# Kernel tuning notes

Measured on AMD Instinct MI355X. Metric: run time of the kernel, lower is better.

Reference implementation:

```python
import jax, jax.numpy as jnp
import numpy as np

B, S, HID = 2, 2048, 1024
NH, HD = 16, 64  # num heads, head dim
NEG = 1e10

def setup_inputs() -> dict:
    key = jax.random.key(0)
    ks = jax.random.split(key, 4)
    scale = 1.0 / np.sqrt(HID)
    return {
        "hidden_states": jax.random.normal(ks[0], (B, S, HID), jnp.float32),
        "attention_mask": jnp.zeros((B, 1, 1, S), jnp.float32),
        "Wq": jax.random.normal(ks[1], (HID, HID), jnp.float32) * scale,
        "bq": jnp.zeros((HID,), jnp.float32),
        "Wk": jax.random.normal(ks[2], (HID, HID), jnp.float32) * scale,
        "bk": jnp.zeros((HID,), jnp.float32),
        "Wv": jax.random.normal(ks[3], (HID, HID), jnp.float32) * scale,
        "bv": jnp.zeros((HID,), jnp.float32),
    }

def _split_heads(x):
    # [B,S,HID] -> [B,NH,S,HD]
    return x.reshape(B, S, NH, HD).transpose(0, 2, 1, 3)

def reference(hidden_states, attention_mask, Wq, bq, Wk, bk, Wv, bv):
    q = _split_heads(hidden_states @ Wq.T + bq)
    k = _split_heads(hidden_states @ Wk.T + bk)
    v = _split_heads(hidden_states @ Wv.T + bv)
    scores = jnp.einsum("bhqd,bhkd->bhqk", q, k) / np.sqrt(HD)
    causal = jnp.tril(jnp.ones((S, S), jnp.float32))  # [S,S]
    scores = scores * causal - NEG * (1.0 - causal)
    scores = scores + attention_mask
    probs = jax.nn.softmax(scores, axis=-1)  # [B,NH,S,S]
    ctx = jnp.einsum("bhqk,bhkd->bhqd", probs, v)
    ctx = ctx.transpose(0, 2, 1, 3).reshape(B, S, HID)
    return (ctx, probs)
```

## Files before the change

kernel.cpp:

```cpp
#include <hip/hip_runtime.h>

#define S_LEN 2048
#define HIDN  1024
#define NHEAD 16
#define HDIM  64
#define NBATCH 2

typedef __bf16 bf16x8 __attribute__((ext_vector_type(8)));
typedef float  f32x4  __attribute__((ext_vector_type(4)));
typedef unsigned int  u32x4 __attribute__((ext_vector_type(4)));
typedef unsigned short u16;
typedef unsigned short u16x4 __attribute__((ext_vector_type(4)));

#define LOG2E      1.4426950408889634f
#define QS_L2E     0.18033688011112042f
#define NEG8_L2E  -11.541560327111707f

#define PSTR 68

__device__ __forceinline__ u16 f2bf(float f) {
    union { float f; unsigned int u; } v; v.f = f;
    unsigned int u = v.u;
    unsigned int r = ((u >> 16) & 1u) + 0x7FFFu;
    return (u16)((u + r) >> 16);
}

__device__ __forceinline__ f32x4 mfma16(bf16x8 a, bf16x8 b, f32x4 c) {
    return __builtin_amdgcn_mfma_f32_16x16x32_bf16(a, b, c, 0, 0, 0);
}

__device__ __forceinline__ f32x4 zf4() { f32x4 z = {0.f, 0.f, 0.f, 0.f}; return z; }

__device__ __forceinline__ bf16x8 pack8_trunc(f32x4 a, f32x4 b) {
    union { f32x4 f; u32x4 u; } ua, ub;
    ua.f = a; ub.f = b;
    union { unsigned int d[4]; bf16x8 v; } r;
    r.d[0] = __builtin_amdgcn_perm(ua.u.y, ua.u.x, 0x07060302u);
    r.d[1] = __builtin_amdgcn_perm(ua.u.w, ua.u.z, 0x07060302u);
    r.d[2] = __builtin_amdgcn_perm(ub.u.y, ub.u.x, 0x07060302u);
    r.d[3] = __builtin_amdgcn_perm(ub.u.w, ub.u.z, 0x07060302u);
    return r.v;
}

__device__ __forceinline__ void gld16(void* lds, const void* g) {
    __builtin_amdgcn_global_load_lds(
        (const __attribute__((address_space(1))) void*)g,
        (__attribute__((address_space(3))) void*)lds, 16, 0, 0);
}

__global__ __launch_bounds__(256) void cvt_bf16(
    const float* __restrict__ s, u16* __restrict__ d, int n)
{
    int i = (blockIdx.x * 256 + threadIdx.x) * 4;
    if (i >= n) return;
    float4 v = *(const float4*)&s[i];
    u16x4 o = { f2bf(v.x), f2bf(v.y), f2bf(v.z), f2bf(v.w) };
    *(u16x4*)&d[i] = o;
}

__global__ __launch_bounds__(256) void qkv_gemm(
    const u16* __restrict__ hsb,
    const u16* __restrict__ Wqb, const u16* __restrict__ Wkb, const u16* __restrict__ Wvb,
    const float* __restrict__ bq, const float* __restrict__ bk, const float* __restrict__ bv,
    u16* __restrict__ Qf, u16* __restrict__ Kf, u16* __restrict__ Vt)
{
    __shared__ u16 As[128 * 32];
    __shared__ u16 Bs[128 * 32];

    const int z = blockIdx.z;
    const u16*   __restrict__ W    = (z == 0) ? Wqb : (z == 1) ? Wkb : Wvb;
    const float* __restrict__ bias = (z == 0) ? bq  : (z == 1) ? bk  : bv;

    const int mbase = blockIdx.x * 128;
    const int nbase = blockIdx.y * 128;
    const int tid  = threadIdx.x;
    const int lane = tid & 63;
    const int wv   = tid >> 6;
    const int wrow = wv >> 1, wcol = wv & 1;
    const int lrow = lane & 15, quad = lane >> 4;

    const int c0 = tid, c1 = tid + 256;
    const int r0 = c0 >> 2, o0 = (c0 & 3) * 8;
    const int r1 = c1 >> 2, o1 = (c1 & 3) * 8;
    const u16* a0p = &hsb[(size_t)(mbase + r0) * HIDN + o0];
    const u16* a1p = &hsb[(size_t)(mbase + r1) * HIDN + o1];
    const u16* b0p = &W  [(size_t)(nbase + r0) * HIDN + o0];
    const u16* b1p = &W  [(size_t)(nbase + r1) * HIDN + o1];

    f32x4 acc[4][4];
#pragma unroll
    for (int i = 0; i < 4; ++i)
#pragma unroll
        for (int j = 0; j < 4; ++j) acc[i][j] = zf4();

    for (int k0 = 0; k0 < HIDN; k0 += 32) {
        gld16(&As[c0 * 8], a0p + k0);
        gld16(&As[c1 * 8], a1p + k0);
        gld16(&Bs[c0 * 8], b0p + k0);
        gld16(&Bs[c1 * 8], b1p + k0);
        __syncthreads();

        bf16x8 af[4], bfr[4];
#pragma unroll
        for (int i = 0; i < 4; ++i)
            af[i] = *(const bf16x8*)&As[(wrow * 64 + i * 16 + lrow) * 32 + quad * 8];
#pragma unroll
        for (int j = 0; j < 4; ++j)
            bfr[j] = *(const bf16x8*)&Bs[(wcol * 64 + j * 16 + lrow) * 32 + quad * 8];
#pragma unroll
        for (int i = 0; i < 4; ++i)
#pragma unroll
            for (int j = 0; j < 4; ++j)
                acc[i][j] = mfma16(af[i], bfr[j], acc[i][j]);
        __syncthreads();
    }

    if (z == 2) {
        const int bb = mbase >> 11;
        const int sb = mbase & 2047;
#pragma unroll
        for (int i = 0; i < 4; ++i) {
#pragma unroll
            for (int j = 0; j < 4; ++j) {
                const int n = nbase + wcol * 64 + j * 16 + lrow;
                const int hh = n >> 6, d = n & 63;
                const float bs = bias[n];
                const int sbase = sb + wrow * 64 + i * 16 + quad * 4;
                u16x4 pk = { f2bf(acc[i][j][0] + bs), f2bf(acc[i][j][1] + bs),
                             f2bf(acc[i][j][2] + bs), f2bf(acc[i][j][3] + bs) };
                *(u16x4*)&Vt[(((size_t)(bb * NHEAD + hh)) * HDIM + d) * S_LEN + sbase] = pk;
            }
        }
    } else {
        u16* __restrict__ O = (z == 0) ? Qf : Kf;
#pragma unroll
        for (int i = 0; i < 4; ++i) {
#pragma unroll
            for (int j = 0; j < 4; ++j) {
                const int n = nbase + wcol * 64 + j * 16 + lrow;
                const float bs = bias[n];
#pragma unroll
                for (int reg = 0; reg < 4; ++reg) {
                    const int m = mbase + wrow * 64 + i * 16 + quad * 4 + reg;
                    O[(size_t)m * HIDN + n] = f2bf(acc[i][j][reg] + bs);
                }
            }
        }
    }
}

__global__ __launch_bounds__(256) void attn_kernel(
    const u16* __restrict__ Qf,
    const u16* __restrict__ Kf,
    const u16* __restrict__ Vt,
    const float* __restrict__ amask,
    float* __restrict__ ctx,
    float* __restrict__ probs)
{
    const int qt = 127 - blockIdx.x;
    const int h  = blockIdx.y;
    const int b  = blockIdx.z;
    const int bh = b * NHEAD + h;
    const int tid  = threadIdx.x;
    const int lane = tid & 63;
    const int wv   = tid >> 6;
    const int lrow = lane & 15, quad = lane >> 4;
    const int row0 = qt * 16;
    const int dti  = qt >> 2;
    const int nkt  = dti + 1;

    __shared__ float pfl[4][16 * PSTR];
    __shared__ float l_sh[4][16];

    {
        const int tail  = nkt * 64;
        const int nt4   = (S_LEN - tail) >> 2;
        const int r  = tid >> 4;
        const int c0 = tid & 15;
        const f32x4 zf = {0.f, 0.f, 0.f, 0.f};
        float* pr = &probs[((size_t)bh * S_LEN + row0 + r) * S_LEN + tail];
        for (int c4 = c0; c4 < nt4; c4 += 16)
            __builtin_nontemporal_store(zf, (f32x4*)&pr[c4 * 4]);
    }

    const u16* qp = &Qf[((size_t)b * S_LEN + row0 + lrow) * HIDN + h * HDIM + quad * 8];
    const bf16x8 qa0 = *(const bf16x8*)qp;
    const bf16x8 qa1 = *(const bf16x8*)(qp + 32);

    const float* __restrict__ am = &amask[(size_t)b * S_LEN];
    const u16* __restrict__ kbase = &Kf[(size_t)b * S_LEN * HIDN + h * HDIM + quad * 8];

    float l_lane[4] = {0.f, 0.f, 0.f, 0.f};
    for (int kt = wv; kt < nkt; kt += 4) {
        f32x4 c[4];
#pragma unroll
        for (int cb = 0; cb < 4; ++cb) {
            const int col = kt * 64 + cb * 16 + lrow;
            const u16* kp = kbase + (size_t)col * HIDN;
            bf16x8 kb0 = *(const bf16x8*)kp;
            bf16x8 kb1 = *(const bf16x8*)(kp + 32);
            c[cb] = mfma16(qa0, kb0, zf4());
            c[cb] = mfma16(qa1, kb1, c[cb]);
        }
        if (kt == dti) {
#pragma unroll
            for (int cb = 0; cb < 4; ++cb) {
                const int col = kt * 64 + cb * 16 + lrow;
                const float m8 = fmaf(am[col], LOG2E, NEG8_L2E);
#pragma unroll
                for (int reg = 0; reg < 4; ++reg) {
                    const int row = row0 + quad * 4 + reg;
                    const float e = exp2f(fmaf(c[cb][reg], QS_L2E, m8));
                    l_lane[reg] += (col <= row) ? e : 0.f;
                }
            }
        } else {
#pragma unroll
            for (int cb = 0; cb < 4; ++cb) {
                const int col = kt * 64 + cb * 16 + lrow;
                const float m8 = fmaf(am[col], LOG2E, NEG8_L2E);
#pragma unroll
                for (int reg = 0; reg < 4; ++reg)
                    l_lane[reg] += exp2f(fmaf(c[cb][reg], QS_L2E, m8));
            }
        }
    }
#pragma unroll
    for (int reg = 0; reg < 4; ++reg) {
#pragma unroll
        for (int off = 1; off < 16; off <<= 1)
            l_lane[reg] += __shfl_xor(l_lane[reg], off, 16);
    }
    if (lrow == 0) {
#pragma unroll
        for (int reg = 0; reg < 4; ++reg)
            l_sh[wv][quad * 4 + reg] = l_lane[reg];
    }
    __syncthreads();
    float inv_l[4];
#pragma unroll
    for (int reg = 0; reg < 4; ++reg) {
        const int rr = quad * 4 + reg;
        inv_l[reg] = 1.f / (l_sh[0][rr] + l_sh[1][rr] + l_sh[2][rr] + l_sh[3][rr]);
    }

    f32x4 av[4];
#pragma unroll
    for (int db = 0; db < 4; ++db) av[db] = zf4();

    float* __restrict__ pw = pfl[wv];
    const u16* __restrict__ vbase = &Vt[(size_t)bh * HDIM * S_LEN + quad * 8];

    for (int kt = wv; kt < nkt; kt += 4) {
        f32x4 c[4];
#pragma unroll
        for (int cb = 0; cb < 4; ++cb) {
            const int col = kt * 64 + cb * 16 + lrow;
            const u16* kp = kbase + (size_t)col * HIDN;
            bf16x8 kb0 = *(const bf16x8*)kp;
            bf16x8 kb1 = *(const bf16x8*)(kp + 32);
            c[cb] = mfma16(qa0, kb0, zf4());
            c[cb] = mfma16(qa1, kb1, c[cb]);
        }
        if (kt == dti) {
#pragma unroll
            for (int cb = 0; cb < 4; ++cb) {
                const int col = kt * 64 + cb * 16 + lrow;
                const float m8 = fmaf(am[col], LOG2E, NEG8_L2E);
#pragma unroll
                for (int reg = 0; reg < 4; ++reg) {
                    const int row = row0 + quad * 4 + reg;
                    const float p = (col <= row)
                        ? exp2f(fmaf(c[cb][reg], QS_L2E, m8)) * inv_l[reg] : 0.f;
                    pw[(quad * 4 + reg) * PSTR + cb * 16 + lrow] = p;
                }
            }
        } else {
#pragma unroll
            for (int cb = 0; cb < 4; ++cb) {
                const int col = kt * 64 + cb * 16 + lrow;
                const float m8 = fmaf(am[col], LOG2E, NEG8_L2E);
#pragma unroll
                for (int reg = 0; reg < 4; ++reg) {
                    const float p = exp2f(fmaf(c[cb][reg], QS_L2E, m8)) * inv_l[reg];
                    pw[(quad * 4 + reg) * PSTR + cb * 16 + lrow] = p;
                }
            }
        }

#pragma unroll
        for (int it = 0; it < 4; ++it) {
            const int r = it * 4 + quad;
            f32x4 v = *(const f32x4*)&pw[r * PSTR + lrow * 4];
            __builtin_nontemporal_store(
                v, (f32x4*)&probs[((size_t)bh * S_LEN + row0 + r) * S_LEN + kt * 64 + lrow * 4]);
        }

        f32x4 p0 = *(const f32x4*)&pw[lrow * PSTR + quad * 8];
        f32x4 p1 = *(const f32x4*)&pw[lrow * PSTR + quad * 8 + 4];
        f32x4 p2 = *(const f32x4*)&pw[lrow * PSTR + 32 + quad * 8];
        f32x4 p3 = *(const f32x4*)&pw[lrow * PSTR + 32 + quad * 8 + 4];
        bf16x8 pa0 = pack8_trunc(p0, p1);
        bf16x8 pa1 = pack8_trunc(p2, p3);
#pragma unroll
        for (int db = 0; db < 4; ++db) {
            const u16* vp = vbase + (size_t)(db * 16 + lrow) * S_LEN + kt * 64;
            bf16x8 vb0 = *(const bf16x8*)vp;
            bf16x8 vb1 = *(const bf16x8*)(vp + 32);
            av[db] = mfma16(pa0, vb0, av[db]);
            av[db] = mfma16(pa1, vb1, av[db]);
        }
    }

#pragma unroll
    for (int db = 0; db < 4; ++db)
#pragma unroll
        for (int reg = 0; reg < 4; ++reg)
            pw[lane * 16 + ((db * 4 + reg + (lane >> 1)) & 15)] = av[db][reg];
    __syncthreads();
#pragma unroll
    for (int reg = 0; reg < 4; ++reg) {
        const int sl = lane * 16 + ((wv * 4 + reg + (lane >> 1)) & 15);
        const float s = pfl[0][sl] + pfl[1][sl] + pfl[2][sl] + pfl[3][sl];
        __builtin_nontemporal_store(
            s, &ctx[((size_t)b * S_LEN + row0 + quad * 4 + reg) * HIDN + h * HDIM + wv * 16 + lrow]);
    }
}

extern "C" void kernel_launch(void* const* d_in, const int* in_sizes, int n_in,
                              void* d_out, int out_size, void* d_ws, size_t ws_size,
                              hipStream_t stream)
{
    const float* hs    = (const float*)d_in[0];
    const float* amask = (const float*)d_in[1];
    const float* Wq    = (const float*)d_in[2];
    const float* bq    = (const float*)d_in[3];
    const float* Wk    = (const float*)d_in[4];
    const float* bk    = (const float*)d_in[5];
    const float* Wv    = (const float*)d_in[6];
    const float* bv    = (const float*)d_in[7];

    float* out   = (float*)d_out;
    float* ctx   = out;
    float* probs = out + (size_t)NBATCH * S_LEN * HIDN;

    const size_t NTOK = (size_t)NBATCH * S_LEN;
    u16* hsb = (u16*)d_ws;
    u16* Wqb = hsb + NTOK * HIDN;
    u16* Wkb = Wqb + (size_t)HIDN * HIDN;
    u16* Wvb = Wkb + (size_t)HIDN * HIDN;
    u16* Qf  = Wvb + (size_t)HIDN * HIDN;
    u16* Kf  = Qf + NTOK * HIDN;
    u16* Vt  = Kf + NTOK * HIDN;

    const int n_hs = (int)(NTOK * HIDN);
    const int n_w  = HIDN * HIDN;
    cvt_bf16<<<n_hs / 1024, 256, 0, stream>>>(hs, hsb, n_hs);
    cvt_bf16<<<n_w  / 1024, 256, 0, stream>>>(Wq, Wqb, n_w);
    cvt_bf16<<<n_w  / 1024, 256, 0, stream>>>(Wk, Wkb, n_w);
    cvt_bf16<<<n_w  / 1024, 256, 0, stream>>>(Wv, Wvb, n_w);

    qkv_gemm<<<dim3(32, 8, 3), 256, 0, stream>>>(hsb, Wqb, Wkb, Wvb, bq, bk, bv, Qf, Kf, Vt);
    attn_kernel<<<dim3(128, 16, 2), 256, 0, stream>>>(Qf, Kf, Vt, amask, ctx, probs);
}
```

Before: 778.9 us.

## Merge conversion launches and widen QKV GEMM K-tile with swizzled LDS and vector stores

Folds the four fp32-to-bf16 conversion launches into a single kernel that picks its source by block index, removing three launch overheads. The QKV GEMM now stages a 64-wide K slice per iteration with an XOR-swizzled LDS layout to avoid bank conflicts. This halves the number of barrier pairs. For Q and K it swaps operand roles so the accumulator holds contiguous output columns, which allows packed 4-element bf16 stores and a float4 bias load instead of scalar strided stores. LDS use doubles, which may reduce occupancy, and the GEMM is small next to the attention kernel, which writes the large probs tensor.

Result: no change. 768.8 us (-1.3%).

```diff
diff --git a/kernel.cpp b/kernel.cpp
--- a/kernel.cpp
+++ b/kernel.cpp
@@ -48,11 +48,21 @@
         (__attribute__((address_space(3))) void*)lds, 16, 0, 0);
 }
 
-__global__ __launch_bounds__(256) void cvt_bf16(
-    const float* __restrict__ s, u16* __restrict__ d, int n)
+__global__ __launch_bounds__(256) void cvt_all(
+    const float* __restrict__ hs, const float* __restrict__ Wq,
+    const float* __restrict__ Wk, const float* __restrict__ Wv,
+    u16* __restrict__ hsb, u16* __restrict__ Wqb,
+    u16* __restrict__ Wkb, u16* __restrict__ Wvb)
 {
-    int i = (blockIdx.x * 256 + threadIdx.x) * 4;
-    if (i >= n) return;
+    const int NBH = (NBATCH * S_LEN * HIDN) / 1024;
+    const int NBW = (HIDN * HIDN) / 1024;
+    int bid = blockIdx.x;
+    const float* __restrict__ s; u16* __restrict__ d;
+    if (bid < NBH)                { s = hs; d = hsb; }
+    else if (bid < NBH + NBW)     { s = Wq; d = Wqb; bid -= NBH; }
+    else if (bid < NBH + 2 * NBW) { s = Wk; d = Wkb; bid -= NBH + NBW; }
+    else                          { s = Wv; d = Wvb; bid -= NBH + 2 * NBW; }
+    const int i = (bid * 256 + (int)threadIdx.x) * 4;
     float4 v = *(const float4*)&s[i];
     u16x4 o = { f2bf(v.x), f2bf(v.y), f2bf(v.z), f2bf(v.w) };
     *(u16x4*)&d[i] = o;
@@ -64,8 +74,8 @@
     const float* __restrict__ bq, const float* __restrict__ bk, const float* __restrict__ bv,
     u16* __restrict__ Qf, u16* __restrict__ Kf, u16* __restrict__ Vt)
 {
-    __shared__ u16 As[128 * 32];
-    __shared__ u16 Bs[128 * 32];
+    __shared__ u16 Rs[128 * 64];
+    __shared__ u16 Cs[128 * 64];
 
     const int z = blockIdx.z;
     const u16*   __restrict__ W    = (z == 0) ? Wqb : (z == 1) ? Wkb : Wvb;
@@ -73,19 +83,27 @@
 
     const int mbase = blockIdx.x * 128;
     const int nbase = blockIdx.y * 128;
+    const u16* __restrict__ Rm = (z == 2) ? hsb : W;
+    const u16* __restrict__ Cm = (z == 2) ? W   : hsb;
+    const int rbase = (z == 2) ? mbase : nbase;
+    const int cbase = (z == 2) ? nbase : mbase;
+
     const int tid  = threadIdx.x;
     const int lane = tid & 63;
     const int wv   = tid >> 6;
     const int wrow = wv >> 1, wcol = wv & 1;
     const int lrow = lane & 15, quad = lane >> 4;
-
-    const int c0 = tid, c1 = tid + 256;
-    const int r0 = c0 >> 2, o0 = (c0 & 3) * 8;
-    const int r1 = c1 >> 2, o1 = (c1 & 3) * 8;
-    const u16* a0p = &hsb[(size_t)(mbase + r0) * HIDN + o0];
-    const u16* a1p = &hsb[(size_t)(mbase + r1) * HIDN + o1];
-    const u16* b0p = &W  [(size_t)(nbase + r0) * HIDN + o0];
-    const u16* b1p = &W  [(size_t)(nbase + r1) * HIDN + o1];
+    const int l7   = lrow & 7;
+
+    const u16* rp[4]; const u16* cp[4];
+#pragma unroll
+    for (int t = 0; t < 4; ++t) {
+        const int c = tid + t * 256;
+        const int r = c >> 3;
+        const int o = ((c & 7) ^ (r & 7)) * 8;
+        rp[t] = &Rm[(size_t)(rbase + r) * HIDN + o];
+        cp[t] = &Cm[(size_t)(cbase + r) * HIDN + o];
+    }
 
     f32x4 acc[4][4];
 #pragma unroll
@@ -93,25 +111,29 @@
 #pragma unroll
         for (int j = 0; j < 4; ++j) acc[i][j] = zf4();
 
-    for (int k0 = 0; k0 < HIDN; k0 += 32) {
-        gld16(&As[c0 * 8], a0p + k0);
-        gld16(&As[c1 * 8], a1p + k0);
-        gld16(&Bs[c0 * 8], b0p + k0);
-        gld16(&Bs[c1 * 8], b1p + k0);
+    for (int k0 = 0; k0 < HIDN; k0 += 64) {
+#pragma unroll
+        for (int t = 0; t < 4; ++t) {
+            gld16(&Rs[(tid + t * 256) * 8], rp[t] + k0);
+            gld16(&Cs[(tid + t * 256) * 8], cp[t] + k0);
+        }
         __syncthreads();
-
-        bf16x8 af[4], bfr[4];
-#pragma unroll
-        for (int i = 0; i < 4; ++i)
-            af[i] = *(const bf16x8*)&As[(wrow * 64 + i * 16 + lrow) * 32 + quad * 8];
-#pragma unroll
-        for (int j = 0; j < 4; ++j)
-            bfr[j] = *(const bf16x8*)&Bs[(wcol * 64 + j * 16 + lrow) * 32 + quad * 8];
-#pragma unroll
-        for (int i = 0; i < 4; ++i)
+#pragma unroll
+        for (int kk = 0; kk < 2; ++kk) {
+            const int sc = ((kk * 4 + quad) ^ l7) * 8;
+            bf16x8 af[4], bfr[4];
+#pragma unroll
+            for (int i = 0; i < 4; ++i)
+                af[i] = *(const bf16x8*)&Rs[(wrow * 64 + i * 16 + lrow) * 64 + sc];
 #pragma unroll
             for (int j = 0; j < 4; ++j)
-                acc[i][j] = mfma16(af[i], bfr[j], acc[i][j]);
+                bfr[j] = *(const bf16x8*)&Cs[(wcol * 64 + j * 16 + lrow) * 64 + sc];
+#pragma unroll
+            for (int i = 0; i < 4; ++i)
+#pragma unroll
+                for (int j = 0; j < 4; ++j)
+                    acc[i][j] = mfma16(af[i], bfr[j], acc[i][j]);
+        }
         __syncthreads();
     }
 
@@ -137,13 +159,12 @@
         for (int i = 0; i < 4; ++i) {
 #pragma unroll
             for (int j = 0; j < 4; ++j) {
-                const int n = nbase + wcol * 64 + j * 16 + lrow;
-                const float bs = bias[n];
-#pragma unroll
-                for (int reg = 0; reg < 4; ++reg) {
-                    const int m = mbase + wrow * 64 + i * 16 + quad * 4 + reg;
-                    O[(size_t)m * HIDN + n] = f2bf(acc[i][j][reg] + bs);
-                }
+                const int n0 = nbase + wrow * 64 + i * 16 + quad * 4;
+                const int m  = mbase + wcol * 64 + j * 16 + lrow;
+                const float4 b4 = *(const float4*)&bias[n0];
+                u16x4 pk = { f2bf(acc[i][j][0] + b4.x), f2bf(acc[i][j][1] + b4.y),
+                             f2bf(acc[i][j][2] + b4.z), f2bf(acc[i][j][3] + b4.w) };
+                *(u16x4*)&O[(size_t)m * HIDN + n0] = pk;
             }
         }
     }
@@ -353,12 +374,8 @@
     u16* Kf  = Qf + NTOK * HIDN;
     u16* Vt  = Kf + NTOK * HIDN;
 
-    const int n_hs = (int)(NTOK * HIDN);
-    const int n_w  = HIDN * HIDN;
-    cvt_bf16<<<n_hs / 1024, 256, 0, stream>>>(hs, hsb, n_hs);
-    cvt_bf16<<<n_w  / 1024, 256, 0, stream>>>(Wq, Wqb, n_w);
-    cvt_bf16<<<n_w  / 1024, 256, 0, stream>>>(Wk, Wkb, n_w);
-    cvt_bf16<<<n_w  / 1024, 256, 0, stream>>>(Wv, Wvb, n_w);
+    const int nblk_cvt = (int)(NTOK * HIDN / 1024) + 3 * (HIDN * HIDN / 1024);
+    cvt_all<<<nblk_cvt, 256, 0, stream>>>(hs, Wq, Wk, Wv, hsb, Wqb, Wkb, Wvb);
 
     qkv_gemm<<<dim3(32, 8, 3), 256, 0, stream>>>(hsb, Wqb, Wkb, Wvb, bq, bk, bv, Qf, Kf, Vt);
     attn_kernel<<<dim3(128, 16, 2), 256, 0, stream>>>(Qf, Kf, Vt, amask, ctx, probs);
```
